# Kernel tuning notes

Hardware: AMD Instinct MI355X
Metric: run time of the kernel (lower is better)

## Reference

```python
import jax, jax.numpy as jnp
import numpy as np

D_MODEL = 2048
NUM_HEADS = 16
HEAD_DIM = D_MODEL // NUM_HEADS
EPS = 1e-6


def setup_inputs() -> dict:
    key = jax.random.key(0)
    ks = jax.random.split(key, 5)
    B, S = 1, 4096
    scale = 1.0 / np.sqrt(D_MODEL)
    return {
        "x": jax.random.normal(ks[0], (B, S, D_MODEL), dtype=jnp.float32),
        "wq": jax.random.normal(ks[1], (D_MODEL, D_MODEL), dtype=jnp.float32) * scale,
        "wk": jax.random.normal(ks[2], (D_MODEL, D_MODEL), dtype=jnp.float32) * scale,
        "wv": jax.random.normal(ks[3], (D_MODEL, D_MODEL), dtype=jnp.float32) * scale,
        "wo": jax.random.normal(ks[4], (D_MODEL, D_MODEL), dtype=jnp.float32) * scale,
        "q_norm_w": jnp.ones((HEAD_DIM,), dtype=jnp.float32),
        "k_norm_w": jnp.ones((HEAD_DIM,), dtype=jnp.float32),
    }


def _rmsnorm(x, w):
    rms = jnp.sqrt(jnp.mean(x * x, axis=-1, keepdims=True) + EPS)
    return x / rms * w


def reference(x, wq, wk, wv, wo, q_norm_w, k_norm_w):
    B, S, _ = x.shape
    # nn.Linear: y = x @ W.T ; split heads -> [B, H, S, Dh]
    def proj(w):
        return (x @ w.T).reshape(B, S, NUM_HEADS, HEAD_DIM).transpose(0, 2, 1, 3)
    q = _rmsnorm(proj(wq), q_norm_w)
    k = _rmsnorm(proj(wk), k_norm_w)
    v = proj(wv)
    scale = 1.0 / np.sqrt(HEAD_DIM)
    attn = jnp.einsum("bhqd,bhkd->bhqk", q, k) * scale  # [B,H,S,S]
    attn = jax.nn.softmax(attn, axis=-1)
    out = jnp.einsum("bhqk,bhkd->bhqd", attn, v)
    out = out.transpose(0, 2, 1, 3).reshape(B, S, D_MODEL)
    return out @ wo.T
```

## Files before the change

### kernel.cpp

```cpp
#include <hip/hip_runtime.h>
#include <hip/hip_bf16.h>

#define S 4096
#define D 2048
#define NH 16
#define HD 128

typedef __attribute__((ext_vector_type(8))) short bf16x8;
typedef __attribute__((ext_vector_type(4))) float f32x4;

typedef __attribute__((address_space(1))) char glob_char;
typedef __attribute__((address_space(3))) char lds_char_t;

__device__ __forceinline__ void gld16(const void* g, void* l) {
    __builtin_amdgcn_global_load_lds((const glob_char*)g, (lds_char_t*)l, 16, 0, 0);
}

__device__ __forceinline__ unsigned short f2b(float f) {
    union { float f; unsigned u; } c; c.f = f;
    unsigned r = c.u + 0x7fff + ((c.u >> 16) & 1);
    return (unsigned short)(r >> 16);
}

__device__ __forceinline__ float fexp2(float x) {
#if __has_builtin(__builtin_amdgcn_exp2f)
    return __builtin_amdgcn_exp2f(x);
#else
    return __expf(x * 0.6931471805599453f);
#endif
}

#define MFMA16(a, b, c) __builtin_amdgcn_mfma_f32_16x16x32_bf16((a), (b), (c), 0, 0, 0)

__global__ __launch_bounds__(256) void cvt_all(
    const float* __restrict__ x,  const float* __restrict__ wq,
    const float* __restrict__ wk, const float* __restrict__ wv,
    const float* __restrict__ wo,
    unsigned short* __restrict__ xb, unsigned short* __restrict__ wqkvb,
    unsigned short* __restrict__ wob)
{
    const int z = blockIdx.y;
    const float* src; unsigned short* dst; int n4;
    if (z == 0)      { src = x;  dst = xb;                        n4 = (S * D) / 4; }
    else if (z == 1) { src = wq; dst = wqkvb;                     n4 = (D * D) / 4; }
    else if (z == 2) { src = wk; dst = wqkvb + (size_t)D * D;     n4 = (D * D) / 4; }
    else if (z == 3) { src = wv; dst = wqkvb + 2 * (size_t)D * D; n4 = (D * D) / 4; }
    else             { src = wo; dst = wob;                       n4 = (D * D) / 4; }
    int i = blockIdx.x * 256 + threadIdx.x;
    if (i < n4) {
        float4 v = ((const float4*)src)[i];
        ushort4 o;
        o.x = f2b(v.x); o.y = f2b(v.y); o.z = f2b(v.z); o.w = f2b(v.w);
        ((ushort4*)dst)[i] = o;
    }
}

template<int OUTMODE>
__global__ __launch_bounds__(512, 2) void gemm8(
    const unsigned short* __restrict__ A, const unsigned short* __restrict__ B,
    void* __restrict__ O0, void* __restrict__ O1, void* __restrict__ O2,
    const float* __restrict__ qw, const float* __restrict__ kw)
{
    __shared__ short lds[65536];
    __shared__ float red[4][256];

    const int tid = threadIdx.x;
    const int lane = tid & 63, col = lane & 15, quad = lane >> 4;
    const int w = tid >> 6, wr = w >> 2, wc = w & 3;
    const int m0 = blockIdx.y * 256, n0 = blockIdx.x * 256;

    const int srow = tid >> 3;
    const int sslot = (tid & 7) ^ (srow & 7);
    const unsigned short* pa0 = A + (size_t)(m0 + srow) * 2048 + sslot * 8;
    const unsigned short* pb0 = B + (size_t)(n0 + srow) * 2048 + sslot * 8;
    const int dst0 = tid * 8;

    auto stA = [&](int t, int h, int buf) {
        const unsigned short* g = pa0 + (size_t)h * 262144 + t * 64;
        short* d = &lds[buf * 16384 + h * 8192 + dst0];
        gld16(g, d);
        gld16(g + 131072, d + 4096);
    };
    auto stB = [&](int t, int h, int buf) {
        const unsigned short* g = pb0 + (size_t)h * 262144 + t * 64;
        short* d = &lds[32768 + buf * 16384 + h * 8192 + dst0];
        gld16(g, d);
        gld16(g + 131072, d + 4096);
    };

    const int sl0 = (quad ^ (col & 7)) << 3;
    const int arow = (wr * 128 + col) * 64;
    const int brow = (wc * 64 + col) * 64;
    auto rdA = [&](int mf, int kk, int buf) -> bf16x8 {
        return *(const bf16x8*)&lds[buf * 16384 + arow + mf * 1024 + (sl0 ^ (kk << 5))];
    };
    auto rdB = [&](int nf, int kk, int buf) -> bf16x8 {
        return *(const bf16x8*)&lds[32768 + buf * 16384 + brow + nf * 1024 + (sl0 ^ (kk << 5))];
    };

    f32x4 acc[8][4];
    #pragma unroll
    for (int i = 0; i < 8; ++i)
        #pragma unroll
        for (int j = 0; j < 4; ++j)
            #pragma unroll
            for (int r = 0; r < 4; ++r) acc[i][j][r] = 0.0f;

    stA(0, 0, 0); stA(0, 1, 0); stB(0, 0, 0); stB(0, 1, 0);
    stA(1, 0, 1); stA(1, 1, 1);
    asm volatile("s_waitcnt vmcnt(4)" ::: "memory");
    __builtin_amdgcn_s_barrier();

    for (int t = 0; t < 32; ++t) {
        const int cur = t & 1, nxt = cur ^ 1;
        const bool s1 = t < 31, s2 = t < 30;
        bf16x8 a0[4][2], a1[4][2], b0[2][2], b1[2][2];

        #pragma unroll
        for (int mf = 0; mf < 4; ++mf) { a0[mf][0] = rdA(mf, 0, cur); a0[mf][1] = rdA(mf, 1, cur); }
        #pragma unroll
        for (int nf = 0; nf < 2; ++nf) { b0[nf][0] = rdB(nf, 0, cur); b0[nf][1] = rdB(nf, 1, cur); }
        if (s1) stB(t + 1, 0, nxt);
        __builtin_amdgcn_s_barrier();
        __builtin_amdgcn_s_setprio(1);
        #pragma unroll
        for (int mf = 0; mf < 4; ++mf)
            #pragma unroll
            for (int nf = 0; nf < 2; ++nf) {
                acc[mf][nf] = MFMA16(a0[mf][0], b0[nf][0], acc[mf][nf]);
                acc[mf][nf] = MFMA16(a0[mf][1], b0[nf][1], acc[mf][nf]);
            }
        __builtin_amdgcn_s_setprio(0);
        __builtin_amdgcn_s_barrier();

        #pragma unroll
        for (int mf = 0; mf < 4; ++mf) { a1[mf][0] = rdA(mf + 4, 0, cur); a1[mf][1] = rdA(mf + 4, 1, cur); }
        #pragma unroll
        for (int nf = 0; nf < 2; ++nf) { b1[nf][0] = rdB(nf + 2, 0, cur); b1[nf][1] = rdB(nf + 2, 1, cur); }
        if (s1) stB(t + 1, 1, nxt);
        __builtin_amdgcn_s_barrier();
        __builtin_amdgcn_s_setprio(1);
        #pragma unroll
        for (int mf = 0; mf < 4; ++mf)
            #pragma unroll
            for (int nf = 0; nf < 2; ++nf) {
                acc[mf][nf + 2] = MFMA16(a0[mf][0], b1[nf][0], acc[mf][nf + 2]);
                acc[mf][nf + 2] = MFMA16(a0[mf][1], b1[nf][1], acc[mf][nf + 2]);
            }
        __builtin_amdgcn_s_setprio(0);
        __builtin_amdgcn_s_barrier();

        if (s2) stA(t + 2, 0, cur);
        __builtin_amdgcn_s_barrier();
        __builtin_amdgcn_s_setprio(1);
        #pragma unroll
        for (int mf = 0; mf < 4; ++mf)
            #pragma unroll
            for (int nf = 0; nf < 2; ++nf) {
                acc[mf + 4][nf] = MFMA16(a1[mf][0], b0[nf][0], acc[mf + 4][nf]);
                acc[mf + 4][nf] = MFMA16(a1[mf][1], b0[nf][1], acc[mf + 4][nf]);
            }
        __builtin_amdgcn_s_setprio(0);
        __builtin_amdgcn_s_barrier();

        if (s2) stA(t + 2, 1, cur);
        __builtin_amdgcn_s_barrier();
        __builtin_amdgcn_s_setprio(1);
        #pragma unroll
        for (int mf = 0; mf < 4; ++mf)
            #pragma unroll
            for (int nf = 0; nf < 2; ++nf) {
                acc[mf + 4][nf + 2] = MFMA16(a1[mf][0], b1[nf][0], acc[mf + 4][nf + 2]);
                acc[mf + 4][nf + 2] = MFMA16(a1[mf][1], b1[nf][1], acc[mf + 4][nf + 2]);
            }
        __builtin_amdgcn_s_setprio(0);
        if (s2)      asm volatile("s_waitcnt vmcnt(4)" ::: "memory");
        else if (s1) asm volatile("s_waitcnt vmcnt(0)" ::: "memory");
        __builtin_amdgcn_s_barrier();
    }

    if (OUTMODE == 1) {
        float* C = (float*)O0;
        #pragma unroll
        for (int mf = 0; mf < 8; ++mf)
            #pragma unroll
            for (int nf = 0; nf < 4; ++nf)
                #pragma unroll
                for (int r = 0; r < 4; ++r)
                    C[(size_t)(m0 + wr * 128 + mf * 16 + quad * 4 + r) * 2048 +
                      n0 + wc * 64 + nf * 16 + col] = acc[mf][nf][r];
    } else {
        const int sel = n0 >> 11;
        if (sel == 2) {
            unsigned short* VtO = (unsigned short*)O2;
            #pragma unroll
            for (int mf = 0; mf < 8; ++mf)
                #pragma unroll
                for (int nf = 0; nf < 4; ++nf) {
                    int n = (n0 & 2047) + wc * 64 + nf * 16 + col;
                    int hh = n >> 7, dv = n & 127;
                    ushort4 pk;
                    pk.x = f2b(acc[mf][nf][0]); pk.y = f2b(acc[mf][nf][1]);
                    pk.z = f2b(acc[mf][nf][2]); pk.w = f2b(acc[mf][nf][3]);
                    *(ushort4*)&VtO[(size_t)hh * (HD * S) + (size_t)dv * S +
                                    m0 + wr * 128 + mf * 16 + quad * 4] = pk;
                }
        } else {
            unsigned short* C = (unsigned short*)(sel == 0 ? O0 : O1);
            const float* wgt = (sel == 0) ? qw : kw;
            const float extra = (sel == 0)
                ? 0.08838834764831845f * 1.4426950408889634f : 1.0f;
            float wv4[4];
            #pragma unroll
            for (int nf = 0; nf < 4; ++nf)
                wv4[nf] = wgt[(wc & 1) * 64 + nf * 16 + col];
            #pragma unroll
            for (int mf = 0; mf < 8; ++mf)
                #pragma unroll
                for (int r = 0; r < 4; ++r) {
                    float ss = 0.0f;
                    #pragma unroll
                    for (int nf = 0; nf < 4; ++nf) ss += acc[mf][nf][r] * acc[mf][nf][r];
                    #pragma unroll
                    for (int d = 1; d < 16; d <<= 1) ss += __shfl_xor(ss, d, 64);
                    if (col == 0) red[wc][wr * 128 + mf * 16 + quad * 4 + r] = ss;
                }
            __syncthreads();
            #pragma unroll
            for (int mf = 0; mf < 8; ++mf) {
                float rsc[4];
                #pragma unroll
                for (int r = 0; r < 4; ++r) {
                    int idx = wr * 128 + mf * 16 + quad * 4 + r;
                    float tot = red[wc & 6][idx] + red[(wc & 6) + 1][idx];
                    rsc[r] = rsqrtf(tot * (1.0f / HD) + 1e-6f) * extra;
                }
                #pragma unroll
                for (int nf = 0; nf < 4; ++nf)
                    #pragma unroll
                    for (int r = 0; r < 4; ++r)
                        C[(size_t)(m0 + wr * 128 + mf * 16 + quad * 4 + r) * 2048 +
                          (n0 & 2047) + wc * 64 + nf * 16 + col] =
                            f2b(acc[mf][nf][r] * rsc[r] * wv4[nf]);
            }
        }
    }
}

struct FlashSmem {
    short Ks[2][8192];
    short Vs[2][8192];
    short Ps[8192];
};

__global__ __launch_bounds__(256, 2) void flash_mfma(
    const unsigned short* __restrict__ Qg, const unsigned short* __restrict__ Kg,
    const unsigned short* __restrict__ Vt, unsigned short* __restrict__ Ctx)
{
    __shared__ FlashSmem sm;

    const int tid = threadIdx.x;
    const int w = tid >> 6, lane = tid & 63, col = lane & 15, quad = lane >> 4;
    const int q0 = blockIdx.x * 128, h = blockIdx.y;

    bf16x8 aq[2][4];
    #pragma unroll
    for (int qs = 0; qs < 2; ++qs) {
        const size_t qoff = (size_t)(q0 + w * 32 + qs * 16 + col) * 2048 + h * 128 + quad * 8;
        #pragma unroll
        for (int ds = 0; ds < 4; ++ds)
            aq[qs][ds] = *(const bf16x8*)&Qg[qoff + ds * 32];
    }

    const unsigned short* kga[4];
    const unsigned short* vga[4];
    #pragma unroll
    for (int it = 0; it < 4; ++it) {
        int c = tid + (it << 8);
        {   int ds = c >> 8, rem = c & 255, key = rem >> 2, ch = rem & 3;
            int g = ch ^ ((key >> 1) & 3);
            kga[it] = &Kg[(size_t)key * 2048 + h * 128 + ds * 32 + g * 8]; }
        {   int ks = c >> 9, rem = c & 511, dv = rem >> 2, ch = rem & 3;
            int g = ch ^ ((dv >> 1) & 3);
            vga[it] = &Vt[(size_t)h * (HD * S) + (size_t)dv * S + ks * 32 + g * 8]; }
    }

    const int fb = col * 32 + ((quad ^ ((col >> 1) & 3)) << 3);
    int ap_off[2][2];
    #pragma unroll
    for (int qs = 0; qs < 2; ++qs) {
        int qrow = w * 32 + qs * 16 + col;
        #pragma unroll
        for (int ks = 0; ks < 2; ++ks) {
            int k0 = ks * 32 + quad * 8;
            ap_off[ks][qs] = qrow * 64 + (k0 ^ ((qrow & 7) << 3));
        }
    }
    int psb2[2][4];
    #pragma unroll
    for (int qs = 0; qs < 2; ++qs)
        #pragma unroll
        for (int r = 0; r < 4; ++r) {
            int ql = w * 32 + qs * 16 + quad * 4 + r;
            int s = (ql & 7) << 3;
            psb2[qs][r] = ql * 64 + (col ^ (s & 8)) + (s & 48);
        }

    bf16x8 vone;
    #pragma unroll
    for (int i = 0; i < 8; ++i) vone[i] = (short)0x3F80;

    f32x4 lacc[2];
    f32x4 o[2][8];
    #pragma unroll
    for (int qs = 0; qs < 2; ++qs) {
        #pragma unroll
        for (int r = 0; r < 4; ++r) lacc[qs][r] = 0.0f;
        #pragma unroll
        for (int nj = 0; nj < 8; ++nj)
            #pragma unroll
            for (int r = 0; r < 4; ++r) o[qs][nj][r] = 0.0f;
    }

    auto stage = [&](int b) {
        #pragma unroll
        for (int it = 0; it < 4; ++it) {
            gld16(kga[it], &sm.Ks[b][(tid + (it << 8)) * 8]);
            kga[it] += 64 * 2048;
        }
        #pragma unroll
        for (int it = 0; it < 4; ++it) {
            gld16(vga[it], &sm.Vs[b][(tid + (it << 8)) * 8]);
            vga[it] += 64;
        }
    };

    auto compute = [&](int b) {
        f32x4 sc[2][4];
        #pragma unroll
        for (int qs = 0; qs < 2; ++qs)
            #pragma unroll
            for (int kj = 0; kj < 4; ++kj)
                #pragma unroll
                for (int r = 0; r < 4; ++r) sc[qs][kj][r] = 0.0f;
        __builtin_amdgcn_s_setprio(1);
        #pragma unroll
        for (int ds = 0; ds < 4; ++ds)
            #pragma unroll
            for (int kj = 0; kj < 4; ++kj) {
                bf16x8 bk = *(const bf16x8*)&sm.Ks[b][fb + ds * 2048 + kj * 512];
                sc[0][kj] = MFMA16(aq[0][ds], bk, sc[0][kj]);
                sc[1][kj] = MFMA16(aq[1][ds], bk, sc[1][kj]);
            }
        __builtin_amdgcn_s_setprio(0);

        #pragma unroll
        for (int qs = 0; qs < 2; ++qs)
            #pragma unroll
            for (int kj = 0; kj < 4; ++kj)
                #pragma unroll
                for (int r = 0; r < 4; ++r)
                    sm.Ps[psb2[qs][r] ^ (kj * 16)] = (short)f2b(fexp2(sc[qs][kj][r]));

        __builtin_amdgcn_s_setprio(1);
        #pragma unroll
        for (int ks = 0; ks < 2; ++ks) {
            bf16x8 ap0 = *(const bf16x8*)&sm.Ps[ap_off[ks][0]];
            bf16x8 ap1 = *(const bf16x8*)&sm.Ps[ap_off[ks][1]];
            lacc[0] = MFMA16(ap0, vone, lacc[0]);
            lacc[1] = MFMA16(ap1, vone, lacc[1]);
            #pragma unroll
            for (int nj = 0; nj < 8; ++nj) {
                bf16x8 bv = *(const bf16x8*)&sm.Vs[b][fb + ks * 4096 + nj * 512];
                o[0][nj] = MFMA16(ap0, bv, o[0][nj]);
                o[1][nj] = MFMA16(ap1, bv, o[1][nj]);
            }
        }
        __builtin_amdgcn_s_setprio(0);
    };

    stage(0);
    for (int j0 = 0; j0 < S; j0 += 128) {
        __syncthreads();
        stage(1);
        compute(0);
        __syncthreads();
        if (j0 + 128 < S) stage(0);
        compute(1);
    }

    #pragma unroll
    for (int qs = 0; qs < 2; ++qs) {
        float inv[4];
        #pragma unroll
        for (int r = 0; r < 4; ++r) inv[r] = 1.0f / lacc[qs][r];
        #pragma unroll
        for (int nj = 0; nj < 8; ++nj)
            #pragma unroll
            for (int r = 0; r < 4; ++r)
                Ctx[(size_t)(q0 + w * 32 + qs * 16 + quad * 4 + r) * 2048 + h * 128 + nj * 16 + col] =
                    f2b(o[qs][nj][r] * inv[r]);
    }
}

extern "C" void kernel_launch(void* const* d_in, const int* in_sizes, int n_in,
                              void* d_out, int out_size, void* d_ws, size_t ws_size,
                              hipStream_t stream)
{
    const float* x  = (const float*)d_in[0];
    const float* wq = (const float*)d_in[1];
    const float* wk = (const float*)d_in[2];
    const float* wv = (const float*)d_in[3];
    const float* wo = (const float*)d_in[4];
    const float* qw = (const float*)d_in[5];
    const float* kw = (const float*)d_in[6];
    float* out = (float*)d_out;

    const size_t MB = 1u << 20;
    char* ws = (char*)d_ws;
    unsigned short* xb    = (unsigned short*)(ws);
    unsigned short* Wqkvb = (unsigned short*)(ws + 16 * MB);
    unsigned short* Wob   = (unsigned short*)(ws + 40 * MB);
    unsigned short* Qb    = (unsigned short*)(ws + 48 * MB);
    unsigned short* Kb    = (unsigned short*)(ws + 64 * MB);
    unsigned short* Vt    = (unsigned short*)(ws + 80 * MB);
    unsigned short* Ctx   = xb;

    cvt_all<<<dim3(8192, 5), dim3(256), 0, stream>>>(x, wq, wk, wv, wo, xb, Wqkvb, Wob);

    gemm8<0><<<dim3(24, 16), dim3(512), 0, stream>>>(xb, Wqkvb, Qb, Kb, Vt, qw, kw);

    flash_mfma<<<dim3(32, 16), dim3(256), 0, stream>>>(Qb, Kb, Vt, Ctx);

    gemm8<1><<<dim3(8, 16), dim3(512), 0, stream>>>(Ctx, Wob, out, out, out, qw, kw);
}
```

Measured before the change: 454.5 us.

## Restructure GEMM k-loop into full-tile double buffering and XCD-aware block remap

```diff
diff --git a/kernel.cpp b/kernel.cpp
--- a/kernel.cpp
+++ b/kernel.cpp
@@ -67,7 +67,12 @@
     const int tid = threadIdx.x;
     const int lane = tid & 63, col = lane & 15, quad = lane >> 4;
     const int w = tid >> 6, wr = w >> 2, wc = w & 3;
-    const int m0 = blockIdx.y * 256, n0 = blockIdx.x * 256;
+
+    const int nwg = gridDim.x * gridDim.y;
+    const int orig = blockIdx.y * gridDim.x + blockIdx.x;
+    const int lin = (orig & 7) * (nwg >> 3) + (orig >> 3);
+    const int m0 = (lin / gridDim.x) * 256;
+    const int n0 = (lin % gridDim.x) * 256;
 
     const int srow = tid >> 3;
     const int sslot = (tid & 7) ^ (srow & 7);
@@ -106,21 +111,12 @@
             #pragma unroll
             for (int r = 0; r < 4; ++r) acc[i][j][r] = 0.0f;
 
-    stA(0, 0, 0); stA(0, 1, 0); stB(0, 0, 0); stB(0, 1, 0);
-    stA(1, 0, 1); stA(1, 1, 1);
-    asm volatile("s_waitcnt vmcnt(4)" ::: "memory");
-    __builtin_amdgcn_s_barrier();
-
-    for (int t = 0; t < 32; ++t) {
-        const int cur = t & 1, nxt = cur ^ 1;
-        const bool s1 = t < 31, s2 = t < 30;
+    auto ktile = [&](int buf, int tst, int mode) {
         bf16x8 a0[4][2], a1[4][2], b0[2][2], b1[2][2];
-
-        #pragma unroll
-        for (int mf = 0; mf < 4; ++mf) { a0[mf][0] = rdA(mf, 0, cur); a0[mf][1] = rdA(mf, 1, cur); }
-        #pragma unroll
-        for (int nf = 0; nf < 2; ++nf) { b0[nf][0] = rdB(nf, 0, cur); b0[nf][1] = rdB(nf, 1, cur); }
-        if (s1) stB(t + 1, 0, nxt);
+        #pragma unroll
+        for (int mf = 0; mf < 4; ++mf) { a0[mf][0] = rdA(mf, 0, buf); a0[mf][1] = rdA(mf, 1, buf); }
+        #pragma unroll
+        for (int nf = 0; nf < 2; ++nf) { b0[nf][0] = rdB(nf, 0, buf); b0[nf][1] = rdB(nf, 1, buf); }
         __builtin_amdgcn_s_barrier();
         __builtin_amdgcn_s_setprio(1);
         #pragma unroll
@@ -134,10 +130,22 @@
         __builtin_amdgcn_s_barrier();
 
         #pragma unroll
-        for (int mf = 0; mf < 4; ++mf) { a1[mf][0] = rdA(mf + 4, 0, cur); a1[mf][1] = rdA(mf + 4, 1, cur); }
-        #pragma unroll
-        for (int nf = 0; nf < 2; ++nf) { b1[nf][0] = rdB(nf + 2, 0, cur); b1[nf][1] = rdB(nf + 2, 1, cur); }
-        if (s1) stB(t + 1, 1, nxt);
+        for (int mf = 0; mf < 4; ++mf) { a1[mf][0] = rdA(mf + 4, 0, buf); a1[mf][1] = rdA(mf + 4, 1, buf); }
+        __builtin_amdgcn_s_barrier();
+        __builtin_amdgcn_s_setprio(1);
+        #pragma unroll
+        for (int mf = 0; mf < 4; ++mf)
+            #pragma unroll
+            for (int nf = 0; nf < 2; ++nf) {
+                acc[mf + 4][nf] = MFMA16(a1[mf][0], b0[nf][0], acc[mf + 4][nf]);
+                acc[mf + 4][nf] = MFMA16(a1[mf][1], b0[nf][1], acc[mf + 4][nf]);
+            }
+        __builtin_amdgcn_s_setprio(0);
+        __builtin_amdgcn_s_barrier();
+
+        #pragma unroll
+        for (int nf = 0; nf < 2; ++nf) { b1[nf][0] = rdB(nf + 2, 0, buf); b1[nf][1] = rdB(nf + 2, 1, buf); }
+        if (mode == 0) { stA(tst, 0, buf); stA(tst, 1, buf); }
         __builtin_amdgcn_s_barrier();
         __builtin_amdgcn_s_setprio(1);
         #pragma unroll
@@ -150,20 +158,7 @@
         __builtin_amdgcn_s_setprio(0);
         __builtin_amdgcn_s_barrier();
 
-        if (s2) stA(t + 2, 0, cur);
-        __builtin_amdgcn_s_barrier();
-        __builtin_amdgcn_s_setprio(1);
-        #pragma unroll
-        for (int mf = 0; mf < 4; ++mf)
-            #pragma unroll
-            for (int nf = 0; nf < 2; ++nf) {
-                acc[mf + 4][nf] = MFMA16(a1[mf][0], b0[nf][0], acc[mf + 4][nf]);
-                acc[mf + 4][nf] = MFMA16(a1[mf][1], b0[nf][1], acc[mf + 4][nf]);
-            }
-        __builtin_amdgcn_s_setprio(0);
-        __builtin_amdgcn_s_barrier();
-
-        if (s2) stA(t + 2, 1, cur);
+        if (mode == 0) { stB(tst, 0, buf); stB(tst, 1, buf); }
         __builtin_amdgcn_s_barrier();
         __builtin_amdgcn_s_setprio(1);
         #pragma unroll
@@ -174,9 +169,21 @@
                 acc[mf + 4][nf + 2] = MFMA16(a1[mf][1], b1[nf][1], acc[mf + 4][nf + 2]);
             }
         __builtin_amdgcn_s_setprio(0);
-        if (s2)      asm volatile("s_waitcnt vmcnt(4)" ::: "memory");
-        else if (s1) asm volatile("s_waitcnt vmcnt(0)" ::: "memory");
-        __builtin_amdgcn_s_barrier();
+        if (mode == 0)      asm volatile("s_waitcnt vmcnt(8)" ::: "memory");
+        else if (mode == 1) asm volatile("s_waitcnt vmcnt(0)" ::: "memory");
+        __builtin_amdgcn_s_barrier();
+    };
+
+    stA(0, 0, 0); stA(0, 1, 0); stB(0, 0, 0); stB(0, 1, 0);
+    stA(1, 0, 1); stA(1, 1, 1); stB(1, 0, 1); stB(1, 1, 1);
+    asm volatile("s_waitcnt vmcnt(8)" ::: "memory");
+    __builtin_amdgcn_s_barrier();
+
+    for (int kt = 0; kt < 16; ++kt) {
+        const int t0 = kt << 1;
+        const bool st = kt < 15;
+        ktile(0, t0 + 2, st ? 0 : 1);
+        ktile(1, t0 + 3, st ? 0 : 2);
     }
 
     if (OUTMODE == 1) {
```

Result: no change. 459.6 us (+1.1%).
